# Performance work log

Hardware: AMD Instinct MI355X
Metric: run time of the kernel (lower is better)

Reference implementation:

```python
import jax, jax.numpy as jnp
import numpy as np

D = 1024  # decoder_hidden_dim


def setup_inputs() -> dict:
    key = jax.random.key(0)
    k1, k2, k3, k4 = jax.random.split(key, 4)
    b, s, d = 32, 2048, D
    decoder_hidden = jax.random.normal(k1, (b, d), dtype=jnp.float32)
    encoder_all_hidden = jax.random.normal(k2, (b, s, d), dtype=jnp.float32)
    # torch nn.Linear(2d, d, bias=False): weight shape (d, 2d)
    W_a = jax.random.normal(k3, (d, 2 * d), dtype=jnp.float32) * (1.0 / np.sqrt(2 * d))
    # torch nn.Linear(d, 1, bias=False): weight shape (1, d) -> store as (d,)
    v = jax.random.normal(k4, (d,), dtype=jnp.float32) * (1.0 / np.sqrt(d))
    return {"decoder_hidden": decoder_hidden, "encoder_all_hidden": encoder_all_hidden,
            "W_a": W_a, "v": v}


def reference(decoder_hidden, encoder_all_hidden, W_a, v):
    d = W_a.shape[0]
    # Split W_a so the (b, s, 2d) concat is never materialized:
    # cat([dec, enc]) @ W_a^T == dec @ Wd^T + enc @ We^T
    Wd = W_a[:, :d]   # acts on decoder part
    We = W_a[:, d:]   # acts on encoder part
    dec_proj = jnp.einsum('bd,ed->be', decoder_hidden, Wd)          # (b, d)
    enc_proj = jnp.einsum('bsd,ed->bse', encoder_all_hidden, We)    # (b, s, d)
    h = jnp.tanh(dec_proj[:, None, :] + enc_proj)                   # (b, s, d)
    scores = jnp.einsum('bse,e->bs', h, v)                          # (b, s)
    alpha = jax.nn.softmax(scores, axis=1)
    return alpha
```

## Files before the change

### kernel.cpp

```cpp
#include <hip/hip_runtime.h>
#include <hip/hip_bf16.h>
#include <stdint.h>


typedef __bf16 bf16x8 __attribute__((ext_vector_type(8)));
typedef __bf16 bf16x2 __attribute__((ext_vector_type(2)));
typedef float floatx4 __attribute__((ext_vector_type(4)));
typedef unsigned short ushort_t;

#define M_TOT 65536
#define D_DIM 1024
#define WA_LD 2048
#define S_DIM 2048

__device__ __forceinline__ unsigned int pack2(float a, float b) {
#if __has_builtin(__builtin_amdgcn_cvt_pk_bf16_f32)
    bf16x2 p = __builtin_amdgcn_cvt_pk_bf16_f32(a, b);
    return __builtin_bit_cast(unsigned int, p);
#else
    unsigned int ua = __float_as_uint(a), ub = __float_as_uint(b);
    ua += 0x7fffu + ((ua >> 16) & 1u);
    ub += 0x7fffu + ((ub >> 16) & 1u);
    return __builtin_amdgcn_perm(ub, ua, 0x07060302);
#endif
}

__device__ __forceinline__ void gl16(const ushort_t* g, ushort_t* l) {
    __builtin_amdgcn_global_load_lds(
        (const __attribute__((address_space(1))) unsigned int*)g,
        (__attribute__((address_space(3))) unsigned int*)l,
        16, 0, 0);
}

__global__ __launch_bounds__(256) void convertW_kernel(
    const float* __restrict__ Wa, ushort_t* __restrict__ Web)
{
    const int e = blockIdx.x;
    const int k = threadIdx.x * 4;
    float4 wv = *(const float4*)(Wa + (size_t)e * WA_LD + D_DIM + k);
    uint2 pk = { pack2(wv.x, wv.y), pack2(wv.z, wv.w) };
    *(uint2*)(Web + (size_t)e * D_DIM + k) = pk;
}

__global__ __launch_bounds__(256) void convert_enc_kernel(
    const float* __restrict__ in, ushort_t* __restrict__ out)
{
    size_t i = ((size_t)blockIdx.x * 256 + threadIdx.x) * 8;
    const size_t stride = (size_t)4096 * 256 * 8;
    for (int it = 0; it < 8; ++it, i += stride) {
        float4 a = *(const float4*)(in + i);
        float4 b = *(const float4*)(in + i + 4);
        uint4 pk = { pack2(a.x, a.y), pack2(a.z, a.w), pack2(b.x, b.y), pack2(b.z, b.w) };
        *(uint4*)(out + i) = pk;
    }
}

__global__ __launch_bounds__(256) void decproj_kernel(
    const float* __restrict__ dec,
    const float* __restrict__ Wa,
    float* __restrict__ dp)
{
    const int b    = blockIdx.y;
    const int wave = threadIdx.x >> 6;
    const int lane = threadIdx.x & 63;
    const int e    = blockIdx.x * 4 + wave;

    __shared__ float s_d[1024];
    for (int t = threadIdx.x; t < 1024; t += 256)
        s_d[t] = dec[b * 1024 + t];
    __syncthreads();

    const float* wrow = Wa + (size_t)e * WA_LD;
    float sum = 0.f;
    #pragma unroll
    for (int k0 = 0; k0 < 1024; k0 += 256) {
        float4 w = *(const float4*)(wrow + k0 + lane * 4);
        float4 d = *(const float4*)(&s_d[k0 + lane * 4]);
        sum += w.x * d.x + w.y * d.y + w.z * d.z + w.w * d.w;
    }
    #pragma unroll
    for (int msk = 1; msk < 64; msk <<= 1)
        sum += __shfl_xor(sum, msk, 64);
    if (lane == 0)
        dp[b * 1024 + e] = sum;
}

__global__ __launch_bounds__(256) void gemm_bf16_kernel(
    const ushort_t* __restrict__ A,
    const ushort_t* __restrict__ Bw,
    const float* __restrict__ v,
    const float* __restrict__ dp,
    float* __restrict__ partial)
{
    __shared__ ushort_t As[128 * 32];
    __shared__ ushort_t Bs[128 * 32];
    __shared__ float s_dec[128], s_v[128], s_score[128];

    const int tid  = threadIdx.x;
    const int lane = tid & 63;
    const int w    = tid >> 6;
    const int wm   = w >> 1;
    const int wn   = w & 1;
    const int r16  = lane & 15;
    const int q    = lane >> 4;

    const int flat    = blockIdx.y * 8 + blockIdx.x;
    const int n_block = (flat >> 3) & 7;
    const int m_block = (flat & 7) | ((flat >> 6) << 3);
    const int b_idx   = m_block >> 4;

    if (tid < 128) {
        s_dec[tid] = dp[b_idx * 1024 + n_block * 128 + tid];
        s_v[tid]   = v[n_block * 128 + tid];
    }

    const int sr = (w << 4) + (lane >> 2);
    const int fS = (sr & 3) ^ ((sr >> 2) & 1);
    const int sg = ((lane & 3) ^ fS) << 3;
    const ushort_t* Ag = A  + (size_t)(m_block * 128 + sr) * D_DIM + sg;
    const ushort_t* Bg = Bw + (size_t)(n_block * 128 + sr) * D_DIM + sg;
    ushort_t* AsW0 = &As[(w << 4) * 32];
    ushort_t* AsW1 = &As[(64 + (w << 4)) * 32];
    ushort_t* BsW0 = &Bs[(w << 4) * 32];
    ushort_t* BsW1 = &Bs[(64 + (w << 4)) * 32];

    const int fR = (r16 & 3) ^ ((r16 >> 2) & 1);
    const int sl = (q ^ fR) << 3;
    const ushort_t* pa[4];
    const ushort_t* pb[4];
    #pragma unroll
    for (int i = 0; i < 4; ++i) {
        pa[i] = &As[(wm * 64 + i * 16 + r16) * 32 + sl];
        pb[i] = &Bs[(wn * 64 + i * 16 + r16) * 32 + sl];
    }

    floatx4 acc[4][4] = {};

    for (int t = 0; t < 32; ++t) {
        const int k0 = t * 32;
        __syncthreads();
        gl16(Ag + k0,              AsW0);
        gl16(Ag + k0 + 64 * D_DIM, AsW1);
        gl16(Bg + k0,              BsW0);
        gl16(Bg + k0 + 64 * D_DIM, BsW1);
        __syncthreads();

        bf16x8 af[4], bfr[4];
        #pragma unroll
        for (int i = 0; i < 4; ++i) af[i]  = *(const bf16x8*)pa[i];
        #pragma unroll
        for (int j = 0; j < 4; ++j) bfr[j] = *(const bf16x8*)pb[j];
        #pragma unroll
        for (int i = 0; i < 4; ++i)
            #pragma unroll
            for (int j = 0; j < 4; ++j)
                acc[i][j] = __builtin_amdgcn_mfma_f32_16x16x32_bf16(af[i], bfr[j], acc[i][j], 0, 0, 0);
    }

    float p[4][4] = {};
    #pragma unroll
    for (int j = 0; j < 4; ++j) {
        const int nl = wn * 64 + j * 16 + r16;
        const float dd = s_dec[nl];
        const float vv = s_v[nl];
        #pragma unroll
        for (int i = 0; i < 4; ++i) {
            #pragma unroll
            for (int r = 0; r < 4; ++r) {
                float x = acc[i][j][r] + dd;
                if (!(x > -8.f)) x = -8.f;
                if (x > 8.f)     x = 8.f;
                float e2 = __expf(2.f * x);
                float h  = 1.f - 2.f * __builtin_amdgcn_rcpf(e2 + 1.f);
                p[i][r] += h * vv;
            }
        }
    }
    #pragma unroll
    for (int msk = 1; msk < 16; msk <<= 1) {
        #pragma unroll
        for (int i = 0; i < 4; ++i)
            #pragma unroll
            for (int r = 0; r < 4; ++r)
                p[i][r] += __shfl_xor(p[i][r], msk, 64);
    }
    __syncthreads();
    if (wn == 0 && r16 == 0) {
        #pragma unroll
        for (int i = 0; i < 4; ++i)
            #pragma unroll
            for (int r = 0; r < 4; ++r)
                s_score[wm * 64 + i * 16 + q * 4 + r] = p[i][r];
    }
    __syncthreads();
    if (wn == 1 && r16 == 0) {
        #pragma unroll
        for (int i = 0; i < 4; ++i)
            #pragma unroll
            for (int r = 0; r < 4; ++r)
                s_score[wm * 64 + i * 16 + q * 4 + r] += p[i][r];
    }
    __syncthreads();
    if (tid < 128)
        partial[(size_t)n_block * M_TOT + m_block * 128 + tid] = s_score[tid];
}

__global__ __launch_bounds__(256) void fused_gemm_fp32_kernel(
    const float* __restrict__ enc,
    const float* __restrict__ Wa,
    const float* __restrict__ v,
    const float* __restrict__ dp,
    float* __restrict__ partial)
{
    __shared__ unsigned short As[128 * 32];
    __shared__ unsigned short Bs[128 * 32];
    __shared__ float s_dec[128];
    __shared__ float s_v[128];
    __shared__ float s_score[128];

    const int tid  = threadIdx.x;
    const int lane = tid & 63;
    const int wave = tid >> 6;
    const int wm   = wave >> 1;
    const int wn   = wave & 1;

    const int flat    = blockIdx.y * 8 + blockIdx.x;
    const int n_block = (flat >> 3) & 7;
    const int m_block = (flat & 7) | ((flat >> 6) << 3);
    const int b_idx   = m_block >> 4;

    if (tid < 128) {
        s_dec[tid] = dp[b_idx * 1024 + n_block * 128 + tid];
        s_v[tid]   = v[n_block * 128 + tid];
    }

    const int r0  = tid >> 2;
    const int kk  = (tid & 3) * 8;
    const int r16 = lane & 15;
    const int q   = lane >> 4;

    const float* A_base = enc + (size_t)m_block * 128 * D_DIM;
    const float* B_base = Wa + (size_t)n_block * 128 * WA_LD + D_DIM;

    floatx4 acc[4][4] = {};

    for (int k0 = 0; k0 < 1024; k0 += 32) {
        float4 a0l = *(const float4*)(A_base + (size_t)r0        * D_DIM + k0 + kk);
        float4 a0h = *(const float4*)(A_base + (size_t)r0        * D_DIM + k0 + kk + 4);
        float4 a1l = *(const float4*)(A_base + (size_t)(r0 + 64) * D_DIM + k0 + kk);
        float4 a1h = *(const float4*)(A_base + (size_t)(r0 + 64) * D_DIM + k0 + kk + 4);
        float4 b0l = *(const float4*)(B_base + (size_t)r0        * WA_LD + k0 + kk);
        float4 b0h = *(const float4*)(B_base + (size_t)r0        * WA_LD + k0 + kk + 4);
        float4 b1l = *(const float4*)(B_base + (size_t)(r0 + 64) * WA_LD + k0 + kk);
        float4 b1h = *(const float4*)(B_base + (size_t)(r0 + 64) * WA_LD + k0 + kk + 4);
        uint4 pa0 = { pack2(a0l.x, a0l.y), pack2(a0l.z, a0l.w), pack2(a0h.x, a0h.y), pack2(a0h.z, a0h.w) };
        uint4 pa1 = { pack2(a1l.x, a1l.y), pack2(a1l.z, a1l.w), pack2(a1h.x, a1h.y), pack2(a1h.z, a1h.w) };
        uint4 pb0 = { pack2(b0l.x, b0l.y), pack2(b0l.z, b0l.w), pack2(b0h.x, b0h.y), pack2(b0h.z, b0h.w) };
        uint4 pb1 = { pack2(b1l.x, b1l.y), pack2(b1l.z, b1l.w), pack2(b1h.x, b1h.y), pack2(b1h.z, b1h.w) };
        __syncthreads();
        *(uint4*)&As[r0        * 32 + kk] = pa0;
        *(uint4*)&As[(r0 + 64) * 32 + kk] = pa1;
        *(uint4*)&Bs[r0        * 32 + kk] = pb0;
        *(uint4*)&Bs[(r0 + 64) * 32 + kk] = pb1;
        __syncthreads();

        bf16x8 af[4], bfr[4];
        #pragma unroll
        for (int i = 0; i < 4; ++i)
            af[i] = *(const bf16x8*)&As[(wm * 64 + i * 16 + r16) * 32 + q * 8];
        #pragma unroll
        for (int j = 0; j < 4; ++j)
            bfr[j] = *(const bf16x8*)&Bs[(wn * 64 + j * 16 + r16) * 32 + q * 8];
        #pragma unroll
        for (int i = 0; i < 4; ++i)
            #pragma unroll
            for (int j = 0; j < 4; ++j)
                acc[i][j] = __builtin_amdgcn_mfma_f32_16x16x32_bf16(af[i], bfr[j], acc[i][j], 0, 0, 0);
    }

    float p[4][4] = {};
    #pragma unroll
    for (int j = 0; j < 4; ++j) {
        const int nl = wn * 64 + j * 16 + r16;
        const float dd = s_dec[nl];
        const float vv = s_v[nl];
        #pragma unroll
        for (int i = 0; i < 4; ++i) {
            #pragma unroll
            for (int r = 0; r < 4; ++r) {
                float x = acc[i][j][r] + dd;
                if (!(x > -8.f)) x = -8.f;
                if (x > 8.f)     x = 8.f;
                float e2 = __expf(2.f * x);
                float h  = 1.f - 2.f * __builtin_amdgcn_rcpf(e2 + 1.f);
                p[i][r] += h * vv;
            }
        }
    }
    #pragma unroll
    for (int msk = 1; msk < 16; msk <<= 1) {
        #pragma unroll
        for (int i = 0; i < 4; ++i)
            #pragma unroll
            for (int r = 0; r < 4; ++r)
                p[i][r] += __shfl_xor(p[i][r], msk, 64);
    }
    __syncthreads();
    if (wn == 0 && r16 == 0) {
        #pragma unroll
        for (int i = 0; i < 4; ++i)
            #pragma unroll
            for (int r = 0; r < 4; ++r)
                s_score[wm * 64 + i * 16 + q * 4 + r] = p[i][r];
    }
    __syncthreads();
    if (wn == 1 && r16 == 0) {
        #pragma unroll
        for (int i = 0; i < 4; ++i)
            #pragma unroll
            for (int r = 0; r < 4; ++r)
                s_score[wm * 64 + i * 16 + q * 4 + r] += p[i][r];
    }
    __syncthreads();
    if (tid < 128)
        partial[(size_t)n_block * M_TOT + m_block * 128 + tid] = s_score[tid];
}

__global__ __launch_bounds__(256) void softmax_kernel(
    const float* __restrict__ partial,
    float* __restrict__ out)
{
    const int b = blockIdx.x;
    const int tid = threadIdx.x;
    __shared__ float wmax[4], wsum[4];

    float sc[8];
    float mx = -1e30f;
    #pragma unroll
    for (int ii = 0; ii < 8; ++ii) {
        const int s = tid + ii * 256;
        float sum = 0.f;
        #pragma unroll
        for (int pp = 0; pp < 8; ++pp)
            sum += partial[(size_t)pp * M_TOT + b * S_DIM + s];
        sc[ii] = sum;
        mx = fmaxf(mx, sum);
    }
    #pragma unroll
    for (int msk = 1; msk < 64; msk <<= 1) mx = fmaxf(mx, __shfl_xor(mx, msk, 64));
    if ((tid & 63) == 0) wmax[tid >> 6] = mx;
    __syncthreads();
    mx = fmaxf(fmaxf(wmax[0], wmax[1]), fmaxf(wmax[2], wmax[3]));

    float ex[8];
    float tot = 0.f;
    #pragma unroll
    for (int ii = 0; ii < 8; ++ii) { ex[ii] = __expf(sc[ii] - mx); tot += ex[ii]; }
    #pragma unroll
    for (int msk = 1; msk < 64; msk <<= 1) tot += __shfl_xor(tot, msk, 64);
    if ((tid & 63) == 0) wsum[tid >> 6] = tot;
    __syncthreads();
    tot = wsum[0] + wsum[1] + wsum[2] + wsum[3];
    const float inv = 1.f / tot;
    #pragma unroll
    for (int ii = 0; ii < 8; ++ii)
        out[b * S_DIM + tid + ii * 256] = ex[ii] * inv;
}

extern "C" void kernel_launch(void* const* d_in, const int* in_sizes, int n_in,
                              void* d_out, int out_size, void* d_ws, size_t ws_size,
                              hipStream_t stream) {
    (void)in_sizes; (void)n_in; (void)out_size;
    const float* dec = (const float*)d_in[0];
    const float* enc = (const float*)d_in[1];
    const float* Wa  = (const float*)d_in[2];
    const float* v   = (const float*)d_in[3];
    float* out = (float*)d_out;

    float* dp      = (float*)d_ws;
    float* partial = dp + 32 * 1024;

    const size_t NEED = (size_t)(32 * 1024 + 8 * 65536) * 4
                      + (size_t)67108864 * 2
                      + (size_t)1048576 * 2;

    if (ws_size >= NEED) {
        ushort_t* encb = (ushort_t*)(partial + 8 * 65536);
        ushort_t* Web  = encb + 67108864;
        convertW_kernel<<<dim3(1024), 256, 0, stream>>>(Wa, Web);
        convert_enc_kernel<<<dim3(4096), 256, 0, stream>>>(enc, encb);
        decproj_kernel<<<dim3(256, 32), 256, 0, stream>>>(dec, Wa, dp);
        gemm_bf16_kernel<<<dim3(8, 512), 256, 0, stream>>>(encb, Web, v, dp, partial);
    } else {
        decproj_kernel<<<dim3(256, 32), 256, 0, stream>>>(dec, Wa, dp);
        fused_gemm_fp32_kernel<<<dim3(8, 512), 256, 0, stream>>>(enc, Wa, v, dp, partial);
    }
    softmax_kernel<<<32, 256, 0, stream>>>(partial, out);
}
```

Baseline: 569.6 us.

## Double-buffer LDS tiles in bf16 GEMM and widen softmax blocks to 1024 threads

The bf16 GEMM main loop now uses two LDS buffers, so the async global-to-LDS load for the next K-slice is issued before computing on the current one. Explicit vmcnt waits, barriers and sched_barriers replace the two __syncthreads per iteration, so the copy overlaps the MFMAs and global latency is hidden. The softmax kernel uses 1024 threads per batch row instead of 256, giving more parallelism across its 32 blocks. The cost is twice the LDS per GEMM block and hand-written wait counts that must match the number of outstanding loads.

```diff
diff --git a/kernel.cpp b/kernel.cpp
--- a/kernel.cpp
+++ b/kernel.cpp
@@ -12,6 +12,11 @@
 #define D_DIM 1024
 #define WA_LD 2048
 #define S_DIM 2048
+
+#define VMCNT4 asm volatile("s_waitcnt vmcnt(4)" ::: "memory")
+#define VMCNT0 asm volatile("s_waitcnt vmcnt(0)" ::: "memory")
+#define BAR    __builtin_amdgcn_s_barrier()
+#define SCHED0 __builtin_amdgcn_sched_barrier(0)
 
 __device__ __forceinline__ unsigned int pack2(float a, float b) {
 #if __has_builtin(__builtin_amdgcn_cvt_pk_bf16_f32)
@@ -85,6 +90,32 @@
         dp[b * 1024 + e] = sum;
 }
 
+__device__ __forceinline__ void stage_step(
+    const ushort_t* Ag, const ushort_t* Bg, int k0,
+    ushort_t* a0, ushort_t* a1, ushort_t* b0, ushort_t* b1)
+{
+    gl16(Ag + k0,              a0);
+    gl16(Ag + k0 + 64 * D_DIM, a1);
+    gl16(Bg + k0,              b0);
+    gl16(Bg + k0 + 64 * D_DIM, b1);
+}
+
+__device__ __forceinline__ void compute_step(
+    const ushort_t* Asb, const ushort_t* Bsb,
+    const int* offA, const int* offB, floatx4 acc[4][4])
+{
+    bf16x8 af[4], bfr[4];
+    #pragma unroll
+    for (int i = 0; i < 4; ++i) af[i]  = *(const bf16x8*)(Asb + offA[i]);
+    #pragma unroll
+    for (int j = 0; j < 4; ++j) bfr[j] = *(const bf16x8*)(Bsb + offB[j]);
+    #pragma unroll
+    for (int i = 0; i < 4; ++i)
+        #pragma unroll
+        for (int j = 0; j < 4; ++j)
+            acc[i][j] = __builtin_amdgcn_mfma_f32_16x16x32_bf16(af[i], bfr[j], acc[i][j], 0, 0, 0);
+}
+
 __global__ __launch_bounds__(256) void gemm_bf16_kernel(
     const ushort_t* __restrict__ A,
     const ushort_t* __restrict__ Bw,
@@ -92,8 +123,8 @@
     const float* __restrict__ dp,
     float* __restrict__ partial)
 {
-    __shared__ ushort_t As[128 * 32];
-    __shared__ ushort_t Bs[128 * 32];
+    __shared__ ushort_t As[2][128 * 32];
+    __shared__ ushort_t Bs[2][128 * 32];
     __shared__ float s_dec[128], s_v[128], s_score[128];
 
     const int tid  = threadIdx.x;
@@ -113,49 +144,45 @@
         s_dec[tid] = dp[b_idx * 1024 + n_block * 128 + tid];
         s_v[tid]   = v[n_block * 128 + tid];
     }
+    __syncthreads();
 
     const int sr = (w << 4) + (lane >> 2);
     const int fS = (sr & 3) ^ ((sr >> 2) & 1);
     const int sg = ((lane & 3) ^ fS) << 3;
     const ushort_t* Ag = A  + (size_t)(m_block * 128 + sr) * D_DIM + sg;
     const ushort_t* Bg = Bw + (size_t)(n_block * 128 + sr) * D_DIM + sg;
-    ushort_t* AsW0 = &As[(w << 4) * 32];
-    ushort_t* AsW1 = &As[(64 + (w << 4)) * 32];
-    ushort_t* BsW0 = &Bs[(w << 4) * 32];
-    ushort_t* BsW1 = &Bs[(64 + (w << 4)) * 32];
+    const int wbase0 = (w << 4) * 32;
+    const int wbase1 = (64 + (w << 4)) * 32;
 
     const int fR = (r16 & 3) ^ ((r16 >> 2) & 1);
     const int sl = (q ^ fR) << 3;
-    const ushort_t* pa[4];
-    const ushort_t* pb[4];
+    int offA[4], offB[4];
     #pragma unroll
     for (int i = 0; i < 4; ++i) {
-        pa[i] = &As[(wm * 64 + i * 16 + r16) * 32 + sl];
-        pb[i] = &Bs[(wn * 64 + i * 16 + r16) * 32 + sl];
+        offA[i] = (wm * 64 + i * 16 + r16) * 32 + sl;
+        offB[i] = (wn * 64 + i * 16 + r16) * 32 + sl;
     }
 
     floatx4 acc[4][4] = {};
 
-    for (int t = 0; t < 32; ++t) {
-        const int k0 = t * 32;
-        __syncthreads();
-        gl16(Ag + k0,              AsW0);
-        gl16(Ag + k0 + 64 * D_DIM, AsW1);
-        gl16(Bg + k0,              BsW0);
-        gl16(Bg + k0 + 64 * D_DIM, BsW1);
-        __syncthreads();
-
-        bf16x8 af[4], bfr[4];
-        #pragma unroll
-        for (int i = 0; i < 4; ++i) af[i]  = *(const bf16x8*)pa[i];
-        #pragma unroll
-        for (int j = 0; j < 4; ++j) bfr[j] = *(const bf16x8*)pb[j];
-        #pragma unroll
-        for (int i = 0; i < 4; ++i)
-            #pragma unroll
-            for (int j = 0; j < 4; ++j)
-                acc[i][j] = __builtin_amdgcn_mfma_f32_16x16x32_bf16(af[i], bfr[j], acc[i][j], 0, 0, 0);
-    }
+    stage_step(Ag, Bg, 0, &As[0][wbase0], &As[0][wbase1], &Bs[0][wbase0], &Bs[0][wbase1]);
+
+    for (int t = 0; t < 30; t += 2) {
+        stage_step(Ag, Bg, (t + 1) * 32, &As[1][wbase0], &As[1][wbase1], &Bs[1][wbase0], &Bs[1][wbase1]);
+        VMCNT4; BAR; SCHED0;
+        compute_step(As[0], Bs[0], offA, offB, acc);
+        SCHED0; BAR;
+        stage_step(Ag, Bg, (t + 2) * 32, &As[0][wbase0], &As[0][wbase1], &Bs[0][wbase0], &Bs[0][wbase1]);
+        VMCNT4; BAR; SCHED0;
+        compute_step(As[1], Bs[1], offA, offB, acc);
+        SCHED0; BAR;
+    }
+    stage_step(Ag, Bg, 31 * 32, &As[1][wbase0], &As[1][wbase1], &Bs[1][wbase0], &Bs[1][wbase1]);
+    VMCNT4; BAR; SCHED0;
+    compute_step(As[0], Bs[0], offA, offB, acc);
+    SCHED0; BAR;
+    VMCNT0; BAR; SCHED0;
+    compute_step(As[1], Bs[1], offA, offB, acc);
 
     float p[4][4] = {};
     #pragma unroll
@@ -326,19 +353,20 @@
         partial[(size_t)n_block * M_TOT + m_block * 128 + tid] = s_score[tid];
 }
 
-__global__ __launch_bounds__(256) void softmax_kernel(
+__global__ __launch_bounds__(1024) void softmax_kernel(
     const float* __restrict__ partial,
     float* __restrict__ out)
 {
     const int b = blockIdx.x;
     const int tid = threadIdx.x;
-    __shared__ float wmax[4], wsum[4];
-
-    float sc[8];
+    const int wv = tid >> 6;
+    __shared__ float wred[16];
+
+    float sc[2];
     float mx = -1e30f;
     #pragma unroll
-    for (int ii = 0; ii < 8; ++ii) {
-        const int s = tid + ii * 256;
+    for (int ii = 0; ii < 2; ++ii) {
+        const int s = tid + ii * 1024;
         float sum = 0.f;
         #pragma unroll
         for (int pp = 0; pp < 8; ++pp)
@@ -348,23 +376,27 @@
     }
     #pragma unroll
     for (int msk = 1; msk < 64; msk <<= 1) mx = fmaxf(mx, __shfl_xor(mx, msk, 64));
-    if ((tid & 63) == 0) wmax[tid >> 6] = mx;
-    __syncthreads();
-    mx = fmaxf(fmaxf(wmax[0], wmax[1]), fmaxf(wmax[2], wmax[3]));
-
-    float ex[8];
+    if ((tid & 63) == 0) wred[wv] = mx;
+    __syncthreads();
+    #pragma unroll
+    for (int k = 0; k < 16; ++k) mx = fmaxf(mx, wred[k]);
+    __syncthreads();
+
+    float ex[2];
     float tot = 0.f;
     #pragma unroll
-    for (int ii = 0; ii < 8; ++ii) { ex[ii] = __expf(sc[ii] - mx); tot += ex[ii]; }
+    for (int ii = 0; ii < 2; ++ii) { ex[ii] = __expf(sc[ii] - mx); tot += ex[ii]; }
     #pragma unroll
     for (int msk = 1; msk < 64; msk <<= 1) tot += __shfl_xor(tot, msk, 64);
-    if ((tid & 63) == 0) wsum[tid >> 6] = tot;
-    __syncthreads();
-    tot = wsum[0] + wsum[1] + wsum[2] + wsum[3];
+    if ((tid & 63) == 0) wred[wv] = tot;
+    __syncthreads();
+    tot = 0.f;
+    #pragma unroll
+    for (int k = 0; k < 16; ++k) tot += wred[k];
     const float inv = 1.f / tot;
     #pragma unroll
-    for (int ii = 0; ii < 8; ++ii)
-        out[b * S_DIM + tid + ii * 256] = ex[ii] * inv;
+    for (int ii = 0; ii < 2; ++ii)
+        out[b * S_DIM + tid + ii * 1024] = ex[ii] * inv;
 }
 
 extern "C" void kernel_launch(void* const* d_in, const int* in_sizes, int n_in,
@@ -395,5 +427,5 @@
         decproj_kernel<<<dim3(256, 32), 256, 0, stream>>>(dec, Wa, dp);
         fused_gemm_fp32_kernel<<<dim3(8, 512), 256, 0, stream>>>(enc, Wa, v, dp, partial);
     }
-    softmax_kernel<<<32, 256, 0, stream>>>(partial, out);
-}
+    softmax_kernel<<<32, 1024, 0, stream>>>(partial, out);
+}
```

Measured after the change: 574.3 us. About the same (+0.8%).
